# Kernel optimization log

Hardware: AMD Instinct MI355X
Metric: run time of the kernel (lower is better)

The kernel has to match this reference:

```python
import jax, jax.numpy as jnp
import numpy as np

LOG2 = 0.6931471805599453

def ssp(x):
    # shifted softplus: softplus(x) - log(2)
    return jax.nn.softplus(x) - LOG2

def residual(v, W, b):
    # PhysNetResidual reuses the same linear twice: linear(act(linear(act(x)))) + x
    h = ssp(v) @ W + b
    h = ssp(h) @ W + b
    return h + v

def setup_inputs() -> dict:
    key = jax.random.key(0)
    ks = jax.random.split(key, 20)
    N, E, D, R = 50000, 600000, 128, 32
    n_int, n_atom_res, n_out_res = 3, 1, 1
    def orth(k, shape):
        return jax.random.orthogonal(k, shape[0])[: shape[0], : shape[1]].astype(jnp.float32) if shape[0] == shape[1] else jax.random.normal(k, shape, jnp.float32) * (1.0 / np.sqrt(shape[0]))
    return {
        "x": jax.random.normal(ks[0], (N, D), jnp.float32),
        "g_ij": jax.random.uniform(ks[1], (E, R), jnp.float32),
        "Wf": orth(ks[2], (D, D)), "bf": jnp.zeros((D,), jnp.float32),
        "Wg": jax.random.normal(ks[3], (R, D), jnp.float32) * (1.0 / np.sqrt(R)),
        "Wj": orth(ks[4], (D, D)), "bj": jnp.zeros((D,), jnp.float32),
        "Wi": orth(ks[5], (D, D)), "bi": jnp.zeros((D,), jnp.float32),
        "u": jnp.ones((D,), jnp.float32),
        "rWint": jnp.stack([orth(ks[6 + i], (D, D)) for i in range(n_int)]),
        "rbint": jnp.zeros((n_int, D), jnp.float32),
        "rWatom": jnp.stack([orth(ks[10 + i], (D, D)) for i in range(n_atom_res)]),
        "rbatom": jnp.zeros((n_atom_res, D), jnp.float32),
        "rWout": jnp.stack([orth(ks[12 + i], (D, D)) for i in range(n_out_res)]),
        "rbout": jnp.zeros((n_out_res, D), jnp.float32),
        "idx_i": jax.random.randint(ks[14], (E,), 0, N, jnp.int32),
        "idx_j": jax.random.randint(ks[15], (E,), 0, N, jnp.int32),
        "n_atoms": N,
    }

def reference(x, g_ij, Wf, bf, Wg, Wj, bj, Wi, bi, u,
              rWint, rbint, rWatom, rbatom, rWout, rbout,
              idx_i, idx_j, n_atoms):
    # --- PhysNetInteraction ---
    xa = ssp(x)                                   # [N, D]
    x_j = xa[idx_j]                               # gather -> [E, D]
    xp = u * xa                                   # [N, D]
    vp = ssp(x_j @ Wj + bj) * (g_ij @ Wg)         # [E, D] RBF-gated messages
    vm = ssp(xa @ Wi + bi)                        # [N, D]
    v = jax.ops.segment_sum(vp, idx_i, num_segments=n_atoms) + vm
    for k in range(rWint.shape[0]):
        v = residual(v, rWint[k], rbint[k])
    v = ssp(v)
    h = xp + v @ Wf + bf                          # [N, D]
    # --- atomic residual stack ---
    for k in range(rWatom.shape[0]):
        h = residual(h, rWatom[k], rbatom[k])
    # --- PhysNetOutput ---
    o = h
    for k in range(rWout.shape[0]):
        o = residual(o, rWout[k], rbout[k])
    o = ssp(o)
    return (o, h)
```

## Files before the change

kernel.cpp:

```cpp
#include <hip/hip_runtime.h>
#include <stdint.h>

#define LOG2F 0.693147180559945f

typedef __attribute__((ext_vector_type(8))) short short8;
typedef __attribute__((ext_vector_type(4))) float f32x4;

__device__ __forceinline__ float ssp(float x){
  float t = __expf(-fabsf(x));
  return fmaxf(x, 0.0f) + __logf(1.0f + t) - LOG2F;
}

__device__ __forceinline__ uint32_t bf16rn(float x){
  uint32_t u = __float_as_uint(x);
  return (u + 0x7fffu + ((u >> 16) & 1u)) >> 16;
}
__device__ __forceinline__ void split2(float x, unsigned short &h, unsigned short &l){
  uint32_t hb = bf16rn(x);
  h = (unsigned short)hb;
  float hf = __uint_as_float(hb << 16);
  l = (unsigned short)bf16rn(x - hf);
}


__global__ __launch_bounds__(256) void k_xconv(
    const float* __restrict__ x, unsigned short* __restrict__ xs, int total)
{
  int i = (blockIdx.x * 256 + threadIdx.x) * 4;
  if (i >= total) return;
  int row = i >> 7, col = i & 127;
  float4 f4 = *(const float4*)(x + i);
  ushort4 h4, l4;
  split2(ssp(f4.x), h4.x, l4.x);
  split2(ssp(f4.y), h4.y, l4.y);
  split2(ssp(f4.z), h4.z, l4.z);
  split2(ssp(f4.w), h4.w, l4.w);
  *(ushort4*)(xs + (size_t)row * 256 + col)       = h4;
  *(ushort4*)(xs + (size_t)row * 256 + 128 + col) = l4;
}

__global__ __launch_bounds__(256) void k_hist(
    const int* __restrict__ idx_i, int* __restrict__ cnt, int E)
{
  int e = blockIdx.x * 256 + threadIdx.x;
  if (e < E) atomicAdd(&cnt[idx_i[e]], 1);
}

__global__ __launch_bounds__(256) void k_scan1(
    int* __restrict__ cnt, int* __restrict__ bsums, int N)
{
  __shared__ int sh[256];
  const int t = threadIdx.x;
  const int base = blockIdx.x * 2048 + t * 8;
  int loc[8], s = 0;
#pragma unroll
  for (int k = 0; k < 8; ++k){
    int v = (base + k < N) ? cnt[base + k] : 0;
    loc[k] = s; s += v;
  }
  sh[t] = s;
  __syncthreads();
  const int own = s;
  for (int off = 1; off < 256; off <<= 1){
    int v = (t >= off) ? sh[t - off] : 0;
    __syncthreads();
    sh[t] += v;
    __syncthreads();
  }
  const int ex = sh[t] - own;
#pragma unroll
  for (int k = 0; k < 8; ++k)
    if (base + k < N) cnt[base + k] = ex + loc[k];
  if (t == 255) bsums[blockIdx.x] = sh[255];
}

__global__ void k_scan2(int* __restrict__ bsums, int nblk){
  if (threadIdx.x == 0 && blockIdx.x == 0){
    int run = 0;
    for (int b = 0; b < nblk; ++b){ int v = bsums[b]; bsums[b] = run; run += v; }
  }
}

__global__ __launch_bounds__(256) void k_scan3(
    int* __restrict__ cnt, const int* __restrict__ bsums, int N)
{
  int i = blockIdx.x * 256 + threadIdx.x;
  if (i < N) cnt[i] += bsums[i >> 11];
}

__global__ __launch_bounds__(256) void k_scatter(
    const int* __restrict__ idx_i, int* __restrict__ ofs,
    int* __restrict__ perm, int E)
{
  int e = blockIdx.x * 256 + threadIdx.x;
  if (e < E){
    int p = atomicAdd(&ofs[idx_i[e]], 1);
    perm[p] = e;
  }
}

__global__ __launch_bounds__(256) void k_wconv(
    const float* __restrict__ Wj, const float* __restrict__ Wg,
    const float* __restrict__ Wi, const float* __restrict__ Wf,
    const float* __restrict__ Wint, const float* __restrict__ Watm,
    const float* __restrict__ Wout,
    unsigned short* __restrict__ ws, int ni, int na, int no)
{
  const int nmat = 3 + ni + na + no;
  int t = blockIdx.x * 256 + threadIdx.x;
  int m = t >> 11, r = t & 2047;
  if (m < nmat){
    const float* src;
    if      (m == 0)           src = Wj;
    else if (m == 1)           src = Wi;
    else if (m <= 1 + ni)      src = Wint + (size_t)(m - 2) * 16384;
    else if (m == 2 + ni)      src = Wf;
    else if (m <= 2 + ni + na) src = Watm + (size_t)(m - 3 - ni) * 16384;
    else                       src = Wout + (size_t)(m - 3 - ni - na) * 16384;
    int lane = r & 63, s = (r >> 6) & 3, ct = r >> 8;
    int col = ct * 16 + (lane & 15);
    int k0  = s * 32 + (lane >> 4) * 8;
    union { unsigned short u[8]; uint4 v; } H, L;
#pragma unroll
    for (int i = 0; i < 8; ++i) split2(src[(size_t)(k0 + i) * 128 + col], H.u[i], L.u[i]);
    ((uint4*)ws)[(size_t)m * 4096 + ((ct * 4 + s) * 2 + 0) * 64 + lane] = H.v;
    ((uint4*)ws)[(size_t)m * 4096 + ((ct * 4 + s) * 2 + 1) * 64 + lane] = L.v;
  } else {
    int uu = t - nmat * 2048;
    if (uu < 512){
      int lane = uu & 63, ct = uu >> 6;
      int col = ct * 16 + (lane & 15);
      int k0  = (lane >> 4) * 8;
      union { unsigned short u8[8]; uint4 v; } H, L;
#pragma unroll
      for (int i = 0; i < 8; ++i) split2(Wg[(size_t)(k0 + i) * 128 + col], H.u8[i], L.u8[i]);
      ((uint4*)ws)[(size_t)nmat * 4096 + (ct * 2 + 0) * 64 + lane] = H.v;
      ((uint4*)ws)[(size_t)nmat * 4096 + (ct * 2 + 1) * 64 + lane] = L.v;
    }
  }
}

__global__ __launch_bounds__(256) void k_edge(
    const unsigned short* __restrict__ xs, const float* __restrict__ g,
    const int* __restrict__ idx_i, const int* __restrict__ idx_j,
    const int* __restrict__ perm,
    const short8* __restrict__ wjf, const short8* __restrict__ wgf,
    const float* __restrict__ bj, float* vacc, int E)
{
  __shared__ __align__(16) char smem[16384 + 4096];
  short8* ahl = (short8*)smem;
  short8* ghl = (short8*)(smem + 16384);
  float*  vp_s = (float*)smem;
  __shared__ int ii_s[32];

  const int t    = threadIdx.x;
  const int lane = t & 63;
  const int w    = t >> 6;
  const int l15  = lane & 15;
  const int lq   = lane >> 4;
  const int e0   = blockIdx.x * 32;

  {
    const int row = t >> 3, kseg = t & 7;
    const int pe = e0 + row;
    const int e = (pe < E) ? perm[pe] : 0;
    const int j = idx_j[e];
    const short8* xp = (const short8*)(xs + (size_t)j * 256);
    const int q0 = kseg * 2;
    short8 fh0 = xp[q0    ];
    short8 fh1 = xp[q0 + 1];
    short8 fl0 = xp[16 + q0    ];
    short8 fl1 = xp[16 + q0 + 1];
    ahl[0*512 + (q0+0)*32 + (row ^ (q0+0))] = fh0;
    ahl[0*512 + (q0+1)*32 + (row ^ (q0+1))] = fh1;
    ahl[1*512 + (q0+0)*32 + (row ^ (q0+0))] = fl0;
    ahl[1*512 + (q0+1)*32 + (row ^ (q0+1))] = fl1;
  }
  if (t < 64){
    const int row = t >> 1, kseg = t & 1;
    const int pe = e0 + row;
    const int e = (pe < E) ? perm[pe] : 0;
    const float4* gp = (const float4*)(g + (size_t)e * 32 + kseg * 16);
    short8 fh0, fh1, fl0, fl1;
#pragma unroll
    for (int q = 0; q < 4; ++q){
      float4 f4 = gp[q];
      float vv[4] = {f4.x, f4.y, f4.z, f4.w};
#pragma unroll
      for (int uu = 0; uu < 4; ++uu){
        unsigned short hh, ll;
        split2(vv[uu], hh, ll);
        int i = q * 4 + uu;
        if (i < 8){ fh0[i]   = (short)hh; fl0[i]   = (short)ll; }
        else      { fh1[i-8] = (short)hh; fl1[i-8] = (short)ll; }
      }
    }
    const int q0 = kseg * 2;
    ghl[0*128 + (q0+0)*32 + (row ^ (q0+0))] = fh0;
    ghl[0*128 + (q0+1)*32 + (row ^ (q0+1))] = fh1;
    ghl[1*128 + (q0+0)*32 + (row ^ (q0+0))] = fl0;
    ghl[1*128 + (q0+1)*32 + (row ^ (q0+1))] = fl1;
  }
  if (t >= 64 && t < 96){
    int rr = t - 64, pe = e0 + rr;
    ii_s[rr] = (pe < E) ? idx_i[perm[pe]] : -1;
  }
  __syncthreads();

  f32x4 am[2][2], ag[2][2];
#pragma unroll
  for (int a = 0; a < 2; ++a)
#pragma unroll
    for (int b = 0; b < 2; ++b){
      am[a][b] = (f32x4){0.f, 0.f, 0.f, 0.f};
      ag[a][b] = (f32x4){0.f, 0.f, 0.f, 0.f};
    }

#pragma unroll
  for (int s = 0; s < 4; ++s){
    const int q = s * 4 + lq;
    short8 a0h = ahl[0*512 + q*32 + ((l15     ) ^ q)];
    short8 a0l = ahl[1*512 + q*32 + ((l15     ) ^ q)];
    short8 a1h = ahl[0*512 + q*32 + ((16 + l15) ^ q)];
    short8 a1l = ahl[1*512 + q*32 + ((16 + l15) ^ q)];
#pragma unroll
    for (int c = 0; c < 2; ++c){
      const int ct = w * 2 + c;
      short8 bh = wjf[((ct*4 + s)*2 + 0)*64 + lane];
      short8 bl = wjf[((ct*4 + s)*2 + 1)*64 + lane];
      am[0][c] = __builtin_amdgcn_mfma_f32_16x16x32_bf16(a0h, bh, am[0][c], 0, 0, 0);
      am[0][c] = __builtin_amdgcn_mfma_f32_16x16x32_bf16(a0h, bl, am[0][c], 0, 0, 0);
      am[0][c] = __builtin_amdgcn_mfma_f32_16x16x32_bf16(a0l, bh, am[0][c], 0, 0, 0);
      am[1][c] = __builtin_amdgcn_mfma_f32_16x16x32_bf16(a1h, bh, am[1][c], 0, 0, 0);
      am[1][c] = __builtin_amdgcn_mfma_f32_16x16x32_bf16(a1h, bl, am[1][c], 0, 0, 0);
      am[1][c] = __builtin_amdgcn_mfma_f32_16x16x32_bf16(a1l, bh, am[1][c], 0, 0, 0);
    }
  }
  {
    const int q = lq;
    short8 g0h = ghl[0*128 + q*32 + ((l15     ) ^ q)];
    short8 g0l = ghl[1*128 + q*32 + ((l15     ) ^ q)];
    short8 g1h = ghl[0*128 + q*32 + ((16 + l15) ^ q)];
    short8 g1l = ghl[1*128 + q*32 + ((16 + l15) ^ q)];
#pragma unroll
    for (int c = 0; c < 2; ++c){
      const int ct = w * 2 + c;
      short8 bh = wgf[(ct*2 + 0)*64 + lane];
      short8 bl = wgf[(ct*2 + 1)*64 + lane];
      ag[0][c] = __builtin_amdgcn_mfma_f32_16x16x32_bf16(g0h, bh, ag[0][c], 0, 0, 0);
      ag[0][c] = __builtin_amdgcn_mfma_f32_16x16x32_bf16(g0h, bl, ag[0][c], 0, 0, 0);
      ag[0][c] = __builtin_amdgcn_mfma_f32_16x16x32_bf16(g0l, bh, ag[0][c], 0, 0, 0);
      ag[1][c] = __builtin_amdgcn_mfma_f32_16x16x32_bf16(g1h, bh, ag[1][c], 0, 0, 0);
      ag[1][c] = __builtin_amdgcn_mfma_f32_16x16x32_bf16(g1h, bl, ag[1][c], 0, 0, 0);
      ag[1][c] = __builtin_amdgcn_mfma_f32_16x16x32_bf16(g1l, bh, ag[1][c], 0, 0, 0);
    }
  }

  __syncthreads();
#pragma unroll
  for (int c = 0; c < 2; ++c){
    const int col = (w * 2 + c) * 16 + l15;
    const float bjv = bj[col];
#pragma unroll
    for (int rt = 0; rt < 2; ++rt)
#pragma unroll
      for (int r = 0; r < 4; ++r){
        const int row = rt * 16 + lq * 4 + r;
        vp_s[row * 132 + col] = ssp(am[rt][c][r] + bjv) * ag[rt][c][r];
      }
  }
  __syncthreads();
  if (t < 128){
    const int col = t;
    float acc = vp_s[col];
    int cur = ii_s[0];
    for (int r = 1; r < 32; ++r){
      const int ii = ii_s[r];
      const float v = vp_s[r * 132 + col];
      if (ii == cur) acc += v;
      else {
        if (cur >= 0) atomicAdd(&vacc[(size_t)cur * 128 + col], acc);
        acc = v; cur = ii;
      }
    }
    if (cur >= 0) atomicAdd(&vacc[(size_t)cur * 128 + col], acc);
  }
}

__global__ __launch_bounds__(256) void k_chain(
    const float* __restrict__ x, const float* vacc,
    const short8* __restrict__ wcf,
    const float* __restrict__ bi, const float* __restrict__ bf_,
    const float* __restrict__ u,
    const float* __restrict__ bint, const float* __restrict__ batm,
    const float* __restrict__ bout,
    float* out, int N, int ni, int na, int no)
{
  __shared__ __align__(16) float arow[32][132];
  __shared__ short8 ahl[1024];

  const int t    = threadIdx.x;
  const int lane = t & 63;
  const int w    = t >> 6;
  const int l15  = lane & 15;
  const int lq   = lane >> 4;
  const int r0   = blockIdx.x * 32;
  const int srow = t >> 3, skseg = t & 7;

  const int col0 = (w*2 + 0)*16 + l15;
  const int col1 = (w*2 + 1)*16 + l15;

  f32x4 am[2][2];

  auto stage = [&](){
    const float* p = &arow[srow][skseg*16];
    short8 fh0, fh1, fl0, fl1;
#pragma unroll
    for (int i = 0; i < 8; ++i){
      unsigned short hh, ll;
      split2(p[i], hh, ll);
      fh0[i] = (short)hh; fl0[i] = (short)ll;
    }
#pragma unroll
    for (int i = 0; i < 8; ++i){
      unsigned short hh, ll;
      split2(p[8+i], hh, ll);
      fh1[i] = (short)hh; fl1[i] = (short)ll;
    }
    const int q0 = skseg * 2;
    ahl[0*512 + (q0+0)*32 + (srow ^ (q0+0))] = fh0;
    ahl[0*512 + (q0+1)*32 + (srow ^ (q0+1))] = fh1;
    ahl[1*512 + (q0+0)*32 + (srow ^ (q0+0))] = fl0;
    ahl[1*512 + (q0+1)*32 + (srow ^ (q0+1))] = fl1;
  };

  auto gemm = [&](const short8* __restrict__ wf){
#pragma unroll
    for (int a = 0; a < 2; ++a)
#pragma unroll
      for (int b = 0; b < 2; ++b) am[a][b] = (f32x4){0.f, 0.f, 0.f, 0.f};
#pragma unroll
    for (int s = 0; s < 4; ++s){
      const int q = s * 4 + lq;
      short8 a0h = ahl[0*512 + q*32 + ((l15     ) ^ q)];
      short8 a0l = ahl[1*512 + q*32 + ((l15     ) ^ q)];
      short8 a1h = ahl[0*512 + q*32 + ((16 + l15) ^ q)];
      short8 a1l = ahl[1*512 + q*32 + ((16 + l15) ^ q)];
#pragma unroll
      for (int c = 0; c < 2; ++c){
        const int ct = w * 2 + c;
        short8 bh = wf[((ct*4 + s)*2 + 0)*64 + lane];
        short8 bl = wf[((ct*4 + s)*2 + 1)*64 + lane];
        am[0][c] = __builtin_amdgcn_mfma_f32_16x16x32_bf16(a0h, bh, am[0][c], 0, 0, 0);
        am[0][c] = __builtin_amdgcn_mfma_f32_16x16x32_bf16(a0h, bl, am[0][c], 0, 0, 0);
        am[0][c] = __builtin_amdgcn_mfma_f32_16x16x32_bf16(a0l, bh, am[0][c], 0, 0, 0);
        am[1][c] = __builtin_amdgcn_mfma_f32_16x16x32_bf16(a1h, bh, am[1][c], 0, 0, 0);
        am[1][c] = __builtin_amdgcn_mfma_f32_16x16x32_bf16(a1h, bl, am[1][c], 0, 0, 0);
        am[1][c] = __builtin_amdgcn_mfma_f32_16x16x32_bf16(a1l, bh, am[1][c], 0, 0, 0);
      }
    }
  };

  auto put_ssp = [&](float (&st)[2][2][4]){
#pragma unroll
    for (int rt = 0; rt < 2; ++rt)
#pragma unroll
      for (int r = 0; r < 4; ++r){
        const int row = rt*16 + lq*4 + r;
        arow[row][col0] = ssp(st[rt][0][r]);
        arow[row][col1] = ssp(st[rt][1][r]);
      }
  };

  auto residual = [&](float (&st)[2][2][4], const short8* wf, const float* bvec){
    const float b0 = bvec[col0], b1 = bvec[col1];
    put_ssp(st);
    __syncthreads();
    stage();
    __syncthreads();
    gemm(wf);
#pragma unroll
    for (int rt = 0; rt < 2; ++rt)
#pragma unroll
      for (int r = 0; r < 4; ++r){
        const int row = rt*16 + lq*4 + r;
        arow[row][col0] = ssp(am[rt][0][r] + b0);
        arow[row][col1] = ssp(am[rt][1][r] + b1);
      }
    __syncthreads();
    stage();
    __syncthreads();
    gemm(wf);
#pragma unroll
    for (int rt = 0; rt < 2; ++rt)
#pragma unroll
      for (int r = 0; r < 4; ++r){
        st[rt][0][r] += am[rt][0][r] + b0;
        st[rt][1][r] += am[rt][1][r] + b1;
      }
  };

  {
    int row = r0 + srow; if (row >= N) row = N - 1;
    const float4* xp = (const float4*)(x + (size_t)row*128 + skseg*16);
    float* p = &arow[srow][skseg*16];
#pragma unroll
    for (int qq = 0; qq < 4; ++qq){
      float4 f4 = xp[qq];
      p[qq*4+0] = ssp(f4.x); p[qq*4+1] = ssp(f4.y);
      p[qq*4+2] = ssp(f4.z); p[qq*4+3] = ssp(f4.w);
    }
    stage();
  }
  __syncthreads();

  float xar[2][2][4];
#pragma unroll
  for (int rt = 0; rt < 2; ++rt)
#pragma unroll
    for (int r = 0; r < 4; ++r){
      const int row = rt*16 + lq*4 + r;
      xar[rt][0][r] = arow[row][col0];
      xar[rt][1][r] = arow[row][col1];
    }

  gemm(wcf + 0);
  float vst[2][2][4];
  {
    const float b0 = bi[col0], b1 = bi[col1];
#pragma unroll
    for (int rt = 0; rt < 2; ++rt)
#pragma unroll
      for (int r = 0; r < 4; ++r){
        int row = r0 + rt*16 + lq*4 + r; if (row >= N) row = N - 1;
        vst[rt][0][r] = vacc[(size_t)row*128 + col0] + ssp(am[rt][0][r] + b0);
        vst[rt][1][r] = vacc[(size_t)row*128 + col1] + ssp(am[rt][1][r] + b1);
      }
  }

  for (int kk = 0; kk < ni; ++kk)
    residual(vst, wcf + (size_t)(1 + kk) * 4096, bint + kk*128);

  put_ssp(vst);
  __syncthreads();
  stage();
  __syncthreads();
  gemm(wcf + (size_t)(1 + ni) * 4096);
  float hst[2][2][4];
  {
    const float b0 = bf_[col0], b1 = bf_[col1];
    const float u0 = u[col0],   u1 = u[col1];
#pragma unroll
    for (int rt = 0; rt < 2; ++rt)
#pragma unroll
      for (int r = 0; r < 4; ++r){
        hst[rt][0][r] = u0 * xar[rt][0][r] + am[rt][0][r] + b0;
        hst[rt][1][r] = u1 * xar[rt][1][r] + am[rt][1][r] + b1;
      }
  }

  for (int kk = 0; kk < na; ++kk)
    residual(hst, wcf + (size_t)(2 + ni + kk) * 4096, batm + kk*128);

#pragma unroll
  for (int rt = 0; rt < 2; ++rt)
#pragma unroll
    for (int r = 0; r < 4; ++r){
      const int row = r0 + rt*16 + lq*4 + r;
      if (row < N){
        out[(size_t)N*128 + (size_t)row*128 + col0] = hst[rt][0][r];
        out[(size_t)N*128 + (size_t)row*128 + col1] = hst[rt][1][r];
      }
    }

  for (int kk = 0; kk < no; ++kk)
    residual(hst, wcf + (size_t)(2 + ni + na + kk) * 4096, bout + kk*128);

#pragma unroll
  for (int rt = 0; rt < 2; ++rt)
#pragma unroll
    for (int r = 0; r < 4; ++r){
      const int row = r0 + rt*16 + lq*4 + r;
      if (row < N){
        out[(size_t)row*128 + col0] = ssp(hst[rt][0][r]);
        out[(size_t)row*128 + col1] = ssp(hst[rt][1][r]);
      }
    }
}

extern "C" void kernel_launch(void* const* d_in, const int* in_sizes, int n_in,
                              void* d_out, int out_size, void* d_ws, size_t ws_size,
                              hipStream_t stream)
{
  const float* x    = (const float*)d_in[0];
  const float* g    = (const float*)d_in[1];
  const float* Wf   = (const float*)d_in[2];
  const float* bf_  = (const float*)d_in[3];
  const float* Wg   = (const float*)d_in[4];
  const float* Wj   = (const float*)d_in[5];
  const float* bj   = (const float*)d_in[6];
  const float* Wi   = (const float*)d_in[7];
  const float* bi   = (const float*)d_in[8];
  const float* u    = (const float*)d_in[9];
  const float* Wint = (const float*)d_in[10];
  const float* bint = (const float*)d_in[11];
  const float* Watm = (const float*)d_in[12];
  const float* batm = (const float*)d_in[13];
  const float* Wout = (const float*)d_in[14];
  const float* bout = (const float*)d_in[15];
  const int* idx_i  = (const int*)d_in[16];
  const int* idx_j  = (const int*)d_in[17];

  const int N  = in_sizes[0] / 128;
  const int E  = in_sizes[16];
  const int ni = in_sizes[10] / 16384;
  const int na = in_sizes[12] / 16384;
  const int no = in_sizes[14] / 16384;

  const int nmat = 3 + ni + na + no;

  float* vacc = (float*)d_out;
  short8* wsf = (short8*)d_ws;
  const short8* wjf = wsf;
  const short8* wcf = wsf + (size_t)1 * 4096;
  const short8* wgf = wsf + (size_t)nmat * 4096;

  const size_t frag_bytes = (size_t)(nmat + 1) * 65536;
  int* cnt   = (int*)((char*)d_ws + frag_bytes);
  int* bsums = cnt + N;
  int* perm  = bsums + 1024;
  char* after = (char*)(perm + E);
  const size_t used = (size_t)(after - (char*)d_ws);
  const size_t xs_bytes = (size_t)N * 256 * sizeof(unsigned short);
  unsigned short* xs = (ws_size >= used + xs_bytes)
      ? (unsigned short*)after
      : (unsigned short*)((float*)d_out + (size_t)N * 128);

  const int nblk = (N + 2047) / 2048;

  hipMemsetAsync(vacc, 0, (size_t)N * 128 * sizeof(float), stream);
  hipMemsetAsync(cnt, 0, (size_t)N * sizeof(int), stream);
  k_xconv  <<<dim3((N*128/4 + 255)/256), dim3(256), 0, stream>>>(x, xs, N * 128);
  k_wconv  <<<dim3((nmat + 1) * 8), dim3(256), 0, stream>>>(Wj, Wg, Wi, Wf, Wint, Watm, Wout,
                                                            (unsigned short*)d_ws, ni, na, no);
  k_hist   <<<dim3((E + 255)/256), dim3(256), 0, stream>>>(idx_i, cnt, E);
  k_scan1  <<<dim3(nblk), dim3(256), 0, stream>>>(cnt, bsums, N);
  k_scan2  <<<dim3(1), dim3(64), 0, stream>>>(bsums, nblk);
  k_scan3  <<<dim3((N + 255)/256), dim3(256), 0, stream>>>(cnt, bsums, N);
  k_scatter<<<dim3((E + 255)/256), dim3(256), 0, stream>>>(idx_i, cnt, perm, E);
  k_edge   <<<dim3((E + 31)/32), dim3(256), 0, stream>>>(xs, g, idx_i, idx_j, perm,
                                                         wjf, wgf, bj, vacc, E);
  k_chain  <<<dim3((N + 31)/32), dim3(256), 0, stream>>>(x, vacc, wcf,
                                                         bi, bf_, u, bint, batm, bout,
                                                         (float*)d_out, N, ni, na, no);
}
```

Before: 535.7 us.

## Write MFMA fragments directly from accumulators with double-buffered LDS; split edge reduction

The chain kernel no longer stages activations through an fp32 row buffer and then re-packs them. Each thread now splits its accumulator values into bf16 hi/lo and writes them straight into the swizzled fragment layout, using two LDS buffers so each GEMM step needs one barrier instead of two. In the edge kernel, the per-column segment reduction moves to a transposed shared layout and is split across all 256 threads, each scanning 16 rows. The cost is more atomics at the half-block boundary and scalar 16-bit LDS stores in place of vector short8 stores.

```diff
diff --git a/kernel.cpp b/kernel.cpp
--- a/kernel.cpp
+++ b/kernel.cpp
@@ -266,24 +266,26 @@
 #pragma unroll
       for (int r = 0; r < 4; ++r){
         const int row = rt * 16 + lq * 4 + r;
-        vp_s[row * 132 + col] = ssp(am[rt][c][r] + bjv) * ag[rt][c][r];
+        vp_s[col * 33 + row] = ssp(am[rt][c][r] + bjv) * ag[rt][c][r];
       }
   }
   __syncthreads();
-  if (t < 128){
-    const int col = t;
-    float acc = vp_s[col];
-    int cur = ii_s[0];
-    for (int r = 1; r < 32; ++r){
-      const int ii = ii_s[r];
-      const float v = vp_s[r * 132 + col];
-      if (ii == cur) acc += v;
+  {
+    const int col = t & 127;
+    const int rbase = (t >> 7) * 16;
+    float acc = 0.f;
+    int curi = -1;
+#pragma unroll
+    for (int r = 0; r < 16; ++r){
+      const int ii = ii_s[rbase + r];
+      const float v = vp_s[col * 33 + rbase + r];
+      if (ii == curi) acc += v;
       else {
-        if (cur >= 0) atomicAdd(&vacc[(size_t)cur * 128 + col], acc);
-        acc = v; cur = ii;
-      }
-    }
-    if (cur >= 0) atomicAdd(&vacc[(size_t)cur * 128 + col], acc);
+        if (curi >= 0) atomicAdd(&vacc[(size_t)curi * 128 + col], acc);
+        acc = v; curi = ii;
+      }
+    }
+    if (curi >= 0) atomicAdd(&vacc[(size_t)curi * 128 + col], acc);
   }
 }
 
@@ -296,8 +298,7 @@
     const float* __restrict__ bout,
     float* out, int N, int ni, int na, int no)
 {
-  __shared__ __align__(16) float arow[32][132];
-  __shared__ short8 ahl[1024];
+  __shared__ short8 ahl[2][1024];
 
   const int t    = threadIdx.x;
   const int lane = t & 63;
@@ -305,36 +306,26 @@
   const int l15  = lane & 15;
   const int lq   = lane >> 4;
   const int r0   = blockIdx.x * 32;
-  const int srow = t >> 3, skseg = t & 7;
 
   const int col0 = (w*2 + 0)*16 + l15;
   const int col1 = (w*2 + 1)*16 + l15;
+  const int q0c = col0 >> 3, e0c = col0 & 7;
+  const int q1c = col1 >> 3, e1c = col1 & 7;
 
   f32x4 am[2][2];
-
-  auto stage = [&](){
-    const float* p = &arow[srow][skseg*16];
-    short8 fh0, fh1, fl0, fl1;
-#pragma unroll
-    for (int i = 0; i < 8; ++i){
-      unsigned short hh, ll;
-      split2(p[i], hh, ll);
-      fh0[i] = (short)hh; fl0[i] = (short)ll;
-    }
-#pragma unroll
-    for (int i = 0; i < 8; ++i){
-      unsigned short hh, ll;
-      split2(p[8+i], hh, ll);
-      fh1[i] = (short)hh; fl1[i] = (short)ll;
-    }
-    const int q0 = skseg * 2;
-    ahl[0*512 + (q0+0)*32 + (srow ^ (q0+0))] = fh0;
-    ahl[0*512 + (q0+1)*32 + (srow ^ (q0+1))] = fh1;
-    ahl[1*512 + (q0+0)*32 + (srow ^ (q0+0))] = fl0;
-    ahl[1*512 + (q0+1)*32 + (srow ^ (q0+1))] = fl1;
+  int cur = 0;
+
+  auto frag_put = [&](int b, int row, int qc, int ec, float v){
+    unsigned short hh, ll;
+    split2(v, hh, ll);
+    unsigned short* base = (unsigned short*)&ahl[b][0];
+    const int idx = (qc*32 + (row ^ qc))*8 + ec;
+    base[idx]        = hh;
+    base[4096 + idx] = ll;
   };
 
   auto gemm = [&](const short8* __restrict__ wf){
+    const short8* A = &ahl[cur][0];
 #pragma unroll
     for (int a = 0; a < 2; ++a)
 #pragma unroll
@@ -342,10 +333,10 @@
 #pragma unroll
     for (int s = 0; s < 4; ++s){
       const int q = s * 4 + lq;
-      short8 a0h = ahl[0*512 + q*32 + ((l15     ) ^ q)];
-      short8 a0l = ahl[1*512 + q*32 + ((l15     ) ^ q)];
-      short8 a1h = ahl[0*512 + q*32 + ((16 + l15) ^ q)];
-      short8 a1l = ahl[1*512 + q*32 + ((16 + l15) ^ q)];
+      short8 a0h = A[0*512 + q*32 + ((l15     ) ^ q)];
+      short8 a0l = A[1*512 + q*32 + ((l15     ) ^ q)];
+      short8 a1h = A[0*512 + q*32 + ((16 + l15) ^ q)];
+      short8 a1l = A[1*512 + q*32 + ((16 + l15) ^ q)];
 #pragma unroll
       for (int c = 0; c < 2; ++c){
         const int ct = w * 2 + c;
@@ -361,35 +352,38 @@
     }
   };
 
-  auto put_ssp = [&](float (&st)[2][2][4]){
+  auto put_ssp_state = [&](float (&st)[2][2][4]){
+    const int b = cur ^ 1;
 #pragma unroll
     for (int rt = 0; rt < 2; ++rt)
 #pragma unroll
       for (int r = 0; r < 4; ++r){
         const int row = rt*16 + lq*4 + r;
-        arow[row][col0] = ssp(st[rt][0][r]);
-        arow[row][col1] = ssp(st[rt][1][r]);
-      }
+        frag_put(b, row, q0c, e0c, ssp(st[rt][0][r]));
+        frag_put(b, row, q1c, e1c, ssp(st[rt][1][r]));
+      }
+    __syncthreads();
+    cur = b;
+  };
+  auto put_ssp_amb = [&](float b0, float b1){
+    const int b = cur ^ 1;
+#pragma unroll
+    for (int rt = 0; rt < 2; ++rt)
+#pragma unroll
+      for (int r = 0; r < 4; ++r){
+        const int row = rt*16 + lq*4 + r;
+        frag_put(b, row, q0c, e0c, ssp(am[rt][0][r] + b0));
+        frag_put(b, row, q1c, e1c, ssp(am[rt][1][r] + b1));
+      }
+    __syncthreads();
+    cur = b;
   };
 
   auto residual = [&](float (&st)[2][2][4], const short8* wf, const float* bvec){
     const float b0 = bvec[col0], b1 = bvec[col1];
-    put_ssp(st);
-    __syncthreads();
-    stage();
-    __syncthreads();
+    put_ssp_state(st);
     gemm(wf);
-#pragma unroll
-    for (int rt = 0; rt < 2; ++rt)
-#pragma unroll
-      for (int r = 0; r < 4; ++r){
-        const int row = rt*16 + lq*4 + r;
-        arow[row][col0] = ssp(am[rt][0][r] + b0);
-        arow[row][col1] = ssp(am[rt][1][r] + b1);
-      }
-    __syncthreads();
-    stage();
-    __syncthreads();
+    put_ssp_amb(b0, b1);
     gemm(wf);
 #pragma unroll
     for (int rt = 0; rt < 2; ++rt)
@@ -400,29 +394,20 @@
       }
   };
 
-  {
-    int row = r0 + srow; if (row >= N) row = N - 1;
-    const float4* xp = (const float4*)(x + (size_t)row*128 + skseg*16);
-    float* p = &arow[srow][skseg*16];
-#pragma unroll
-    for (int qq = 0; qq < 4; ++qq){
-      float4 f4 = xp[qq];
-      p[qq*4+0] = ssp(f4.x); p[qq*4+1] = ssp(f4.y);
-      p[qq*4+2] = ssp(f4.z); p[qq*4+3] = ssp(f4.w);
-    }
-    stage();
-  }
+  float xar[2][2][4];
+#pragma unroll
+  for (int rt = 0; rt < 2; ++rt)
+#pragma unroll
+    for (int r = 0; r < 4; ++r){
+      int row = r0 + rt*16 + lq*4 + r; if (row >= N) row = N - 1;
+      const int lrow = rt*16 + lq*4 + r;
+      float v0 = ssp(x[(size_t)row*128 + col0]);
+      float v1 = ssp(x[(size_t)row*128 + col1]);
+      xar[rt][0][r] = v0; xar[rt][1][r] = v1;
+      frag_put(0, lrow, q0c, e0c, v0);
+      frag_put(0, lrow, q1c, e1c, v1);
+    }
   __syncthreads();
-
-  float xar[2][2][4];
-#pragma unroll
-  for (int rt = 0; rt < 2; ++rt)
-#pragma unroll
-    for (int r = 0; r < 4; ++r){
-      const int row = rt*16 + lq*4 + r;
-      xar[rt][0][r] = arow[row][col0];
-      xar[rt][1][r] = arow[row][col1];
-    }
 
   gemm(wcf + 0);
   float vst[2][2][4];
@@ -441,10 +426,7 @@
   for (int kk = 0; kk < ni; ++kk)
     residual(vst, wcf + (size_t)(1 + kk) * 4096, bint + kk*128);
 
-  put_ssp(vst);
-  __syncthreads();
-  stage();
-  __syncthreads();
+  put_ssp_state(vst);
   gemm(wcf + (size_t)(1 + ni) * 4096);
   float hst[2][2][4];
   {
```

Measured after the change: 533.4 us. No clear change (-0.4%).
